# Optimization experiments

Measured on AMD Instinct MI355X. Metric: run time of the kernel, lower is better.

Reference implementation:

```python
import jax, jax.numpy as jnp
import numpy as np

B = 4096
N = 8192
LEVEL_SIZES = [8, 128, 2048, 6008]  # sums to N; 4-level taxonomy
EPS = 1e-07


def _build_hierarchy():
    """parent[c] = parent node index (-1 for roots); level_of[c] = depth."""
    rng = np.random.default_rng(0)
    parent = np.full(N, -1, np.int32)
    level_of = np.zeros(N, np.int32)
    off, prev_start, prev_size = 0, 0, 0
    for l, sz in enumerate(LEVEL_SIZES):
        level_of[off:off + sz] = l
        if l > 0:
            parent[off:off + sz] = rng.integers(prev_start, prev_start + prev_size, sz)
        prev_start, prev_size = off, sz
        off += sz
    return parent, level_of


def setup_inputs() -> dict:
    key = jax.random.key(0)
    k1, k2 = jax.random.split(key)
    pred = jax.random.normal(k1, (B, N), dtype=jnp.float32)  # logits
    target = (jax.random.uniform(k2, (B, N)) < 0.02).astype(jnp.float32)
    parent_np, level_np = _build_hierarchy()
    return {
        "pred": pred,
        "target": target,
        "parent": jnp.asarray(parent_np),
        "level_of": jnp.asarray(level_np),
        "mode": 0,  # 0 = EVAL (propagate conditional probs), 1 = TRAIN
    }


def reference(pred, target, parent, level_of, mode):
    p = jax.nn.sigmoid(pred)                      # [B, N]
    parent_clip = jnp.maximum(parent, 0)          # safe gather index for roots
    is_root = parent < 0                          # recursive_relation[-1]

    if mode != 1:  # not 'TRAIN': top-down conditional probability propagation
        pc = p
        for l in range(1, len(LEVEL_SIZES)):
            # pred_clone[:, children(n)] = pred[:, children] * pred_clone[:, n]
            pc = jnp.where(level_of == l, p * pc[:, parent_clip], pc)
        pred_clone = pc
    else:
        pred_clone = None

    # mask[b, c] = 1 if c is a root, or if target[b, parent[c]] == 1
    mask = jnp.where(is_root, jnp.float32(1.0), target[:, parent_clip])

    pcl = jnp.clip(p, EPS, 1.0 - EPS)
    loss = -(jnp.log(pcl) * target + (1.0 - target) * mask * jnp.log(1.0 - pcl))
    loss = loss.sum(axis=1).mean()
    return (loss, pred_clone)
```

## Files before the change

kernel.cpp:

```cpp
#include <hip/hip_runtime.h>


typedef float f4 __attribute__((ext_vector_type(4)));
typedef float f2 __attribute__((ext_vector_type(2)));
typedef int   i4 __attribute__((ext_vector_type(4)));

#define N_NODES 8192
#define L1S 8
#define L2S 136
#define L3S 2184
#define N4   2048
#define L3S4 546

__device__ __forceinline__ float frcp(float x) { return __builtin_amdgcn_rcpf(x); }

__global__ __launch_bounds__(256, 8) void cs_main(
    const float* __restrict__ pred,
    const float* __restrict__ target,
    const int* __restrict__ parent,
    float* __restrict__ out,
    float* __restrict__ bsum,
    float inv_b)
{
    __shared__ float pk[L3S];
    __shared__ float red[4];

    const int tid = threadIdx.x;
    const int lane = tid & 63;
    const int b = blockIdx.x;
    const float* __restrict__ prow = pred + (size_t)b * N_NODES;
    const float* __restrict__ trow = target + (size_t)b * N_NODES;
    float* __restrict__ orow = out + 1 + (size_t)b * N_NODES;
    const f4* __restrict__ Pp = (const f4*)prow;
    const f4* __restrict__ Tp = (const f4*)trow;
    const i4* __restrict__ Qp = (const i4*)parent;

    f4 ax[3], at[3];
#pragma unroll
    for (int k = 0; k < 3; ++k) {
        const int g = min(tid + k * 256, L3S4 - 1);
        ax[k] = Pp[g]; at[k] = Tp[g];
    }
#pragma unroll
    for (int k = 0; k < 3; ++k) {
        const int g = tid + k * 256;
        if (g < L3S4) {
            f4 v;
#pragma unroll
            for (int j = 0; j < 4; ++j) {
                const float p = frcp(1.0f + __expf(-ax[k][j]));
                v[j] = at[k][j] > 0.5f ? -p : p;
            }
            *(f4*)(pk + 4 * g) = v;
        }
    }
    __syncthreads();

    float lsum = 0.0f;
#pragma unroll
    for (int k = 0; k < 9; ++k) {
        const int c = tid + k * 256;
        if (c < L3S) {
            const float v = pk[c];
            const float p = fabsf(v);
            const bool t = (v < 0.0f);
            float mask, cum;
            if (c < L1S) {
                mask = 1.0f; cum = p;
            } else {
                const int pa = parent[c];
                const float pv = pk[pa];
                mask = (pv < 0.0f) ? 1.0f : 0.0f;
                if (c < L2S) {
                    cum = p * fabsf(pv);
                } else {
                    const float gv = pk[parent[pa]];
                    cum = p * fabsf(pv) * fabsf(gv);
                    pk[c] = t ? -cum : cum;
                }
            }
            lsum += t ? -__logf(p) : mask * (-__logf(1.0f - p));
            orow[c] = cum;
        }
    }
    __syncthreads();

    int g = L3S4 + tid;
    f4 xA = Pp[g], tA = Tp[g]; i4 qA = Qp[g];
    {
        const int g1 = g + 256;
        f4 xB = Pp[g1], tB = Tp[g1]; i4 qB = Qp[g1];
#pragma unroll
        for (int k = 0; k < 6; ++k) {
            f4 nx, nt; i4 nq;
            if (k < 4) {
                const int gp = min(g + 512, N4 - 1);
                nx = Pp[gp]; nt = Tp[gp]; nq = Qp[gp];
            }
            if (g < N4) {
                float rr[4];
#pragma unroll
                for (int j = 0; j < 4; ++j) {
                    const float x = xA[j], t = tA[j];
                    const float pv = pk[qA[j]];
                    const float mask = (pv < 0.0f) ? 1.0f : 0.0f;
                    const float e = __expf(-x);
                    const float s = __logf(1.0f + e);
                    const float p = frcp(1.0f + e);
                    lsum += t * s + (1.0f - t) * mask * (s + x);
                    rr[j] = p * fabsf(pv);
                }
                const float prev3 = __shfl_up(rr[3], 1);
                float* slot = out + (size_t)b * N_NODES + 4 * g;
                if (lane >= 4) {
                    f4 v = {prev3, rr[0], rr[1], rr[2]};
                    __builtin_nontemporal_store(v, (f4*)slot);
                } else if (lane > 0) {
                    *(f4*)slot = f4{prev3, rr[0], rr[1], rr[2]};
                } else {
                    slot[1] = rr[0];
                    *(f2*)(slot + 2) = f2{rr[1], rr[2]};
                }
                if (lane == 63 || g == N4 - 1) slot[4] = rr[3];
            }
            xA = xB; tA = tB; qA = qB;
            xB = nx; tB = nt; qB = nq;
            g += 256;
        }
    }

#pragma unroll
    for (int off = 32; off > 0; off >>= 1) lsum += __shfl_down(lsum, off);
    if (lane == 0) red[tid >> 6] = lsum;
    __syncthreads();
    if (tid == 0) {
        const float s = (red[0] + red[1]) + (red[2] + red[3]);
        if (bsum) bsum[b] = s;
        else atomicAdd(out, s * inv_b);
    }
}

__global__ __launch_bounds__(256) void cs_finish(
    const float* __restrict__ bsum, float* __restrict__ out,
    int n, float inv_b)
{
    __shared__ float red[4];
    const int tid = threadIdx.x;
    float s = 0.0f;
    for (int i = tid; i < n; i += 256) s += bsum[i];
#pragma unroll
    for (int off = 32; off > 0; off >>= 1) s += __shfl_down(s, off);
    if ((tid & 63) == 0) red[tid >> 6] = s;
    __syncthreads();
    if (tid == 0) out[0] = ((red[0] + red[1]) + (red[2] + red[3])) * inv_b;
}

extern "C" void kernel_launch(void* const* d_in, const int* in_sizes, int n_in,
                              void* d_out, int out_size, void* d_ws, size_t ws_size,
                              hipStream_t stream) {
    const float* pred   = (const float*)d_in[0];
    const float* target = (const float*)d_in[1];
    const int*   parent = (const int*)d_in[2];

    float* out = (float*)d_out;
    const int batch = in_sizes[0] / N_NODES;
    const float inv_b = 1.0f / (float)batch;

    if (ws_size >= (size_t)batch * sizeof(float)) {
        float* bsum = (float*)d_ws;
        cs_main<<<batch, 256, 0, stream>>>(pred, target, parent, out, bsum, inv_b);
        cs_finish<<<1, 256, 0, stream>>>(bsum, out, batch, inv_b);
    } else {
        hipMemsetAsync(d_out, 0, sizeof(float), stream);
        cs_main<<<batch, 256, 0, stream>>>(pred, target, parent, out, nullptr, inv_b);
    }
}
```

Measured before the change: 104.3 us.

## Vectorize early-level pass, drop block reduction sync, retune launch bounds

```diff
diff --git a/kernel.cpp b/kernel.cpp
--- a/kernel.cpp
+++ b/kernel.cpp
@@ -14,7 +14,7 @@
 
 __device__ __forceinline__ float frcp(float x) { return __builtin_amdgcn_rcpf(x); }
 
-__global__ __launch_bounds__(256, 8) void cs_main(
+__global__ __launch_bounds__(256, 6) void cs_main(
     const float* __restrict__ pred,
     const float* __restrict__ target,
     const int* __restrict__ parent,
@@ -23,64 +23,82 @@
     float inv_b)
 {
     __shared__ float pk[L3S];
-    __shared__ float red[4];
 
     const int tid = threadIdx.x;
     const int lane = tid & 63;
     const int b = blockIdx.x;
     const float* __restrict__ prow = pred + (size_t)b * N_NODES;
     const float* __restrict__ trow = target + (size_t)b * N_NODES;
-    float* __restrict__ orow = out + 1 + (size_t)b * N_NODES;
+    float* __restrict__ obase = out + (size_t)b * N_NODES;
     const f4* __restrict__ Pp = (const f4*)prow;
     const f4* __restrict__ Tp = (const f4*)trow;
     const i4* __restrict__ Qp = (const i4*)parent;
 
-    f4 ax[3], at[3];
+    f4 ax[3];
+    {
+        f4 at[3];
 #pragma unroll
-    for (int k = 0; k < 3; ++k) {
-        const int g = min(tid + k * 256, L3S4 - 1);
-        ax[k] = Pp[g]; at[k] = Tp[g];
-    }
+        for (int k = 0; k < 3; ++k) {
+            const int g = min(tid + k * 256, L3S4 - 1);
+            ax[k] = Pp[g]; at[k] = Tp[g];
+        }
 #pragma unroll
-    for (int k = 0; k < 3; ++k) {
-        const int g = tid + k * 256;
-        if (g < L3S4) {
-            f4 v;
+        for (int k = 0; k < 3; ++k) {
+            const int g = tid + k * 256;
+            if (g < L3S4) {
+                f4 v;
 #pragma unroll
-            for (int j = 0; j < 4; ++j) {
-                const float p = frcp(1.0f + __expf(-ax[k][j]));
-                v[j] = at[k][j] > 0.5f ? -p : p;
+                for (int j = 0; j < 4; ++j) {
+                    const float p = frcp(1.0f + __expf(-ax[k][j]));
+                    v[j] = at[k][j] > 0.5f ? -p : p;
+                }
+                *(f4*)(pk + 4 * g) = v;
             }
-            *(f4*)(pk + 4 * g) = v;
         }
     }
     __syncthreads();
 
     float lsum = 0.0f;
+
 #pragma unroll
-    for (int k = 0; k < 9; ++k) {
-        const int c = tid + k * 256;
-        if (c < L3S) {
-            const float v = pk[c];
-            const float p = fabsf(v);
-            const bool t = (v < 0.0f);
-            float mask, cum;
-            if (c < L1S) {
-                mask = 1.0f; cum = p;
-            } else {
-                const int pa = parent[c];
-                const float pv = pk[pa];
-                mask = (pv < 0.0f) ? 1.0f : 0.0f;
-                if (c < L2S) {
+    for (int k = 0; k < 3; ++k) {
+        const int g = tid + k * 256;
+        if (g < L3S4) {
+            const f4 v = *(const f4*)(pk + 4 * g);
+            const i4 q = Qp[g];
+            f4 cums;
+#pragma unroll
+            for (int j = 0; j < 4; ++j) {
+                const float p = fabsf(v[j]);
+                const float tf = (v[j] < 0.0f) ? 1.0f : 0.0f;
+                float mf, cum;
+                if (g < L1S / 4) {
+                    mf = 1.0f; cum = p;
+                } else if (g < L2S / 4) {
+                    const float pv = pk[q[j]];
+                    mf = (pv < 0.0f) ? 1.0f : 0.0f;
                     cum = p * fabsf(pv);
                 } else {
-                    const float gv = pk[parent[pa]];
+                    const float pv = pk[q[j]];
+                    const float gv = pk[parent[q[j]]];
+                    mf = (pv < 0.0f) ? 1.0f : 0.0f;
                     cum = p * fabsf(pv) * fabsf(gv);
-                    pk[c] = t ? -cum : cum;
+                    pk[4 * g + j] = (tf > 0.0f) ? -cum : cum;
                 }
+                const float s = -__logf(p);
+                const float cx = mf - tf * mf;
+                lsum += (tf + cx) * s + cx * ax[k][j];
+                cums[j] = cum;
             }
-            lsum += t ? -__logf(p) : mask * (-__logf(1.0f - p));
-            orow[c] = cum;
+            const float prev3 = __shfl_up(cums[3], 1);
+            float* slot = obase + 4 * g;
+            if (lane > 0) {
+                *(f4*)slot = f4{prev3, cums[0], cums[1], cums[2]};
+            } else {
+                slot[1] = cums[0];
+                *(f2*)(slot + 2) = f2{cums[1], cums[2]};
+            }
+            if (lane == 63 || g == L3S4 - 1) slot[4] = cums[3];
         }
     }
     __syncthreads();
@@ -98,24 +116,22 @@
                 nx = Pp[gp]; nt = Tp[gp]; nq = Qp[gp];
             }
             if (g < N4) {
-                float rr[4];
+                f4 rr;
 #pragma unroll
                 for (int j = 0; j < 4; ++j) {
-                    const float x = xA[j], t = tA[j];
+                    const float x = xA[j], tf = tA[j];
                     const float pv = pk[qA[j]];
-                    const float mask = (pv < 0.0f) ? 1.0f : 0.0f;
+                    const float mf = (pv < 0.0f) ? 1.0f : 0.0f;
                     const float e = __expf(-x);
                     const float s = __logf(1.0f + e);
                     const float p = frcp(1.0f + e);
-                    lsum += t * s + (1.0f - t) * mask * (s + x);
+                    const float cx = mf - tf * mf;
+                    lsum += (tf + cx) * s + cx * x;
                     rr[j] = p * fabsf(pv);
                 }
                 const float prev3 = __shfl_up(rr[3], 1);
-                float* slot = out + (size_t)b * N_NODES + 4 * g;
-                if (lane >= 4) {
-                    f4 v = {prev3, rr[0], rr[1], rr[2]};
-                    __builtin_nontemporal_store(v, (f4*)slot);
-                } else if (lane > 0) {
+                float* slot = obase + 4 * g;
+                if (lane > 0) {
                     *(f4*)slot = f4{prev3, rr[0], rr[1], rr[2]};
                 } else {
                     slot[1] = rr[0];
@@ -131,23 +147,23 @@
 
 #pragma unroll
     for (int off = 32; off > 0; off >>= 1) lsum += __shfl_down(lsum, off);
-    if (lane == 0) red[tid >> 6] = lsum;
-    __syncthreads();
-    if (tid == 0) {
-        const float s = (red[0] + red[1]) + (red[2] + red[3]);
-        if (bsum) bsum[b] = s;
-        else atomicAdd(out, s * inv_b);
+    if (lane == 0) {
+        if (bsum) bsum[b * 4 + (tid >> 6)] = lsum;
+        else atomicAdd(out, lsum * inv_b);
     }
 }
 
 __global__ __launch_bounds__(256) void cs_finish(
     const float* __restrict__ bsum, float* __restrict__ out,
-    int n, float inv_b)
+    int n4, float inv_b)
 {
     __shared__ float red[4];
     const int tid = threadIdx.x;
     float s = 0.0f;
-    for (int i = tid; i < n; i += 256) s += bsum[i];
+    for (int i = tid; i < n4; i += 256) {
+        const f4 v = ((const f4*)bsum)[i];
+        s += (v[0] + v[1]) + (v[2] + v[3]);
+    }
 #pragma unroll
     for (int off = 32; off > 0; off >>= 1) s += __shfl_down(s, off);
     if ((tid & 63) == 0) red[tid >> 6] = s;
@@ -166,7 +182,7 @@
     const int batch = in_sizes[0] / N_NODES;
     const float inv_b = 1.0f / (float)batch;
 
-    if (ws_size >= (size_t)batch * sizeof(float)) {
+    if (ws_size >= (size_t)batch * 4 * sizeof(float)) {
         float* bsum = (float*)d_ws;
         cs_main<<<batch, 256, 0, stream>>>(pred, target, parent, out, bsum, inv_b);
         cs_finish<<<1, 256, 0, stream>>>(bsum, out, batch, inv_b);
```

Result: faster. 89.40 us (median of 2 runs) (-14.3%).
